# Kernel optimization log

Hardware: AMD Instinct MI355X
Metric: run time of the kernel (lower is better)

Reference implementation:

```python
import jax, jax.numpy as jnp
import numpy as np

ALL_NODE_NUM = 12288
FEA_DIM = 32           # dim2 in DGATNet
BATCH_SIZE = 8
WIN_NUM = 4
POOLED_PER_WIN = 192   # ratio=0.5 of 384 nodes per window graph
N_EDGES = 393216       # avg degree 32


def setup_inputs() -> dict:
    key = jax.random.key(0)
    k1, k2, k3, k4, k5 = jax.random.split(key, 5)
    n_perm = BATCH_SIZE * WIN_NUM * POOLED_PER_WIN  # 6144
    fea = jax.random.normal(k1, (n_perm, FEA_DIM), dtype=jnp.float32)
    # perm: unique sorted node indices kept by the pooling stage
    perm = jnp.sort(jax.random.permutation(k2, ALL_NODE_NUM)[:n_perm]).astype(jnp.int32)
    encoder_edge_index = jax.random.randint(k3, (2, N_EDGES), 0, ALL_NODE_NUM, dtype=jnp.int32)
    encoder_edge_attr = jax.random.uniform(k4, (N_EDGES,), dtype=jnp.float32)
    node_atte_coffe = jax.random.uniform(k5, (BATCH_SIZE * POOLED_PER_WIN,), dtype=jnp.float32)
    return {
        "fea": fea,
        "perm": perm,
        "encoder_edge_index": encoder_edge_index,
        "encoder_edge_attr": encoder_edge_attr,
        "node_atte_coffe": node_atte_coffe,
        "all_node_num": ALL_NODE_NUM,
        "batch_size": BATCH_SIZE,
    }


def reference(fea, perm, encoder_edge_index, encoder_edge_attr, node_atte_coffe,
              all_node_num, batch_size):
    """Faithful JAX translation of DiffusioUnpool.forward (DGATNet.unpool)."""
    n_perm, fea_dim = fea.shape
    slide_win_num = n_perm // node_atte_coffe.shape[0]
    node_num = node_atte_coffe.shape[0] // batch_size

    # ones(B,W,1) @ coffe(B,1,node_num) == tile coefficients over windows
    nac = node_atte_coffe.reshape(batch_size, 1, node_num)
    win_nac = jnp.broadcast_to(nac, (batch_size, slide_win_num, node_num)).reshape(-1)

    # scatter pooled features / coefficients back into the full node set
    x_zero = jnp.zeros((all_node_num, fea_dim), dtype=fea.dtype).at[perm].set(fea)
    atte_zero = jnp.zeros((all_node_num,), dtype=fea.dtype).at[perm].set(win_nac)

    # dense adjacency (duplicate edges sum, as in sparse_coo_tensor + to_dense)
    A = jnp.zeros((all_node_num, all_node_num), dtype=fea.dtype)
    A = A.at[encoder_edge_index[0], encoder_edge_index[1]].add(encoder_edge_attr)
    A = A + jnp.eye(all_node_num, dtype=fea.dtype)  # + I self loops

    d = 1.0 / jnp.sqrt(jnp.sum(A, axis=1))  # diag of D = deg^{-1/2}
    # D A D x  ==  d * (A @ (d * x))
    x = d[:, None] * (A @ (d[:, None] * x_zero))
    atte_updata = d * (A @ (d * atte_zero))
    return x, atte_updata
```

## Files before the change

kernel.cpp:

```cpp
#include <hip/hip_runtime.h>

constexpr int ALL_NODES = 12288;
constexpr int FEA       = 32;
constexpr int N_PERM    = 6144;
constexpr int N_EDGES   = 393216;
constexpr int NODE_NUM  = 192;
constexpr int WINxNODE  = 768;

constexpr int RCAP   = 48;
constexpr int NWORDS = ALL_NODES / 32;

constexpr size_t ROWBUF_OFF = 0;
constexpr size_t YC_OFF   = ROWBUF_OFF + (size_t)ALL_NODES * RCAP * 2;
constexpr size_t CNT_OFF  = YC_OFF + (size_t)N_PERM * FEA;
constexpr size_t DEG_OFF  = CNT_OFF + ALL_NODES;
constexpr size_t DV_OFF   = DEG_OFF + ALL_NODES;
constexpr size_t YA_OFF   = DV_OFF + ALL_NODES;
constexpr size_t BMP_OFF  = YA_OFF + N_PERM;
constexpr size_t RANK_OFF = BMP_OFF + NWORDS;

__global__ __launch_bounds__(512) void k_init(const int* __restrict__ perm,
                                              unsigned int* __restrict__ cnt,
                                              float* __restrict__ deg,
                                              unsigned int* __restrict__ bmp,
                                              int* __restrict__ rank) {
    int t = threadIdx.x;
    if (blockIdx.x == 0) {
        __shared__ int pops[NWORDS];
        unsigned bits = 0u;
        if (t < NWORDS) {
            int base = t * 32;
            int loI = 0, hiI = N_PERM;
            while (loI < hiI) {
                int mid = (loI + hiI) >> 1;
                if (perm[mid] < base) loI = mid + 1; else hiI = mid;
            }
            for (int k = loI; k < N_PERM; ++k) {
                int p = perm[k];
                if (p >= base + 32) break;
                bits |= 1u << (p - base);
            }
            bmp[t] = bits;
            pops[t] = __popc(bits);
        }
        __syncthreads();
        for (int off = 1; off < NWORDS; off <<= 1) {
            int v = 0;
            if (t < NWORDS && t >= off) v = pops[t - off];
            __syncthreads();
            if (t < NWORDS) pops[t] += v;
            __syncthreads();
        }
        if (t < NWORDS) rank[t] = pops[t] - __popc(bits);
    } else {
        int z = (blockIdx.x - 1) * 512 + t;
        if (z < ALL_NODES) cnt[z] = 0u;
        else deg[z - ALL_NODES] = 0.f;
    }
}

__global__ __launch_bounds__(256) void k_bin(const int* __restrict__ ei0,
                                             const int* __restrict__ ei1,
                                             const float* __restrict__ attr,
                                             const unsigned int* __restrict__ bmp,
                                             const int* __restrict__ rank,
                                             float* __restrict__ deg,
                                             unsigned int* __restrict__ cnt,
                                             uint2* __restrict__ rowbuf) {
    int e = blockIdx.x * 256 + threadIdx.x;
    int r = ei0[e];
    int c = ei1[e];
    float w = attr[e];
    atomicAdd(&deg[r], w);
    unsigned word = bmp[c >> 5];
    if ((word >> (c & 31)) & 1u) {
        int kk = rank[c >> 5] + __popc(word & ((1u << (c & 31)) - 1u));
        unsigned slot = atomicAdd(&cnt[r], 1u);
        if (slot < RCAP)
            rowbuf[(size_t)r * RCAP + slot] =
                make_uint2((unsigned)kk, __float_as_uint(w));
    }
}

__global__ __launch_bounds__(256) void k_post(const float* __restrict__ fea,
                                              const float* __restrict__ nac,
                                              const float* __restrict__ deg,
                                              const unsigned int* __restrict__ bmp,
                                              const int* __restrict__ rank,
                                              float* __restrict__ dv,
                                              float* __restrict__ yc,
                                              float* __restrict__ ya) {
    int tg = blockIdx.x * 256 + threadIdx.x;
    int i = tg >> 3, s = tg & 7;
    float d = rsqrtf(1.0f + deg[i]);
    if (s == 0) dv[i] = d;
    unsigned word = bmp[i >> 5];
    if ((word >> (i & 31)) & 1u) {
        int kk = rank[i >> 5] + __popc(word & ((1u << (i & 31)) - 1u));
        float4 v = *(const float4*)(fea + (size_t)kk * FEA + s * 4);
        v.x *= d; v.y *= d; v.z *= d; v.w *= d;
        ((float4*)yc)[(size_t)kk * 8 + s] = v;
        if (s == 0)
            ya[kk] = d * nac[(kk / WINxNODE) * NODE_NUM + (kk % NODE_NUM)];
    }
}

__global__ __launch_bounds__(256) void k_spmv(const uint2* __restrict__ rowbuf,
                                              const unsigned int* __restrict__ cnt,
                                              const float* __restrict__ dv,
                                              const float* __restrict__ yc,
                                              const float* __restrict__ ya,
                                              const unsigned int* __restrict__ bmp,
                                              const int* __restrict__ rank,
                                              float* __restrict__ out_x,
                                              float* __restrict__ out_a) {
    int t = threadIdx.x;
    int r = blockIdx.x * 8 + (t >> 5);
    int f = t & 31;
    int n = (int)cnt[r]; if (n > RCAP) n = RCAP;
    const uint2* rp = rowbuf + (size_t)r * RCAP;
    float acc = 0.f, accA = 0.f;
    int i = 0;
    for (; i + 4 <= n; i += 4) {
        uint2 e0 = rp[i],     e1 = rp[i + 1];
        uint2 e2 = rp[i + 2], e3 = rp[i + 3];
        float y0 = yc[(size_t)e0.x * FEA + f];
        float y1 = yc[(size_t)e1.x * FEA + f];
        float y2 = yc[(size_t)e2.x * FEA + f];
        float y3 = yc[(size_t)e3.x * FEA + f];
        acc += __uint_as_float(e0.y) * y0 + __uint_as_float(e1.y) * y1
             + __uint_as_float(e2.y) * y2 + __uint_as_float(e3.y) * y3;
        if (f == 0)
            accA += __uint_as_float(e0.y) * ya[e0.x]
                  + __uint_as_float(e1.y) * ya[e1.x]
                  + __uint_as_float(e2.y) * ya[e2.x]
                  + __uint_as_float(e3.y) * ya[e3.x];
    }
    for (; i < n; ++i) {
        uint2 e = rp[i];
        acc += __uint_as_float(e.y) * yc[(size_t)e.x * FEA + f];
        if (f == 0) accA += __uint_as_float(e.y) * ya[e.x];
    }
    float d = dv[r];
    unsigned word = bmp[r >> 5];
    float self = 0.f, selfa = 0.f;
    if ((word >> (r & 31)) & 1u) {
        int kk = rank[r >> 5] + __popc(word & ((1u << (r & 31)) - 1u));
        self  = yc[(size_t)kk * FEA + f];
        selfa = ya[kk];
    }
    out_x[(size_t)r * FEA + f] = d * (acc + self);
    if (f == 0)
        out_a[r] = d * (accA + selfa);
}

extern "C" void kernel_launch(void* const* d_in, const int* in_sizes, int n_in,
                              void* d_out, int out_size, void* d_ws, size_t ws_size,
                              hipStream_t stream) {
    const float* fea  = (const float*)d_in[0];
    const int*   perm = (const int*)d_in[1];
    const int*   ei   = (const int*)d_in[2];
    const float* attr = (const float*)d_in[3];
    const float* nac  = (const float*)d_in[4];

    unsigned int* ws     = (unsigned int*)d_ws;
    uint2*        rowbuf = (uint2*)(ws + ROWBUF_OFF);
    float*        yc     = (float*)(ws + YC_OFF);
    unsigned int* cnt    = ws + CNT_OFF;
    float*        deg    = (float*)(ws + DEG_OFF);
    float*        dv     = (float*)(ws + DV_OFF);
    float*        ya     = (float*)(ws + YA_OFF);
    unsigned int* bmp    = ws + BMP_OFF;
    int*          rank   = (int*)(ws + RANK_OFF);

    float* out_x = (float*)d_out;
    float* out_a = out_x + ALL_NODES * FEA;

    k_init<<<49,            512, 0, stream>>>(perm, cnt, deg, bmp, rank);
    k_bin <<<N_EDGES / 256, 256, 0, stream>>>(ei, ei + N_EDGES, attr, bmp, rank,
                                              deg, cnt, rowbuf);
    k_post<<<384,           256, 0, stream>>>(fea, nac, deg, bmp, rank, dv, yc, ya);
    k_spmv<<<ALL_NODES / 8, 256, 0, stream>>>(rowbuf, cnt, dv, yc, ya, bmp, rank,
                                              out_x, out_a);
}
```

Measured before the change: 120.6 us.

## Pack degree and slot count into one 64-bit atomic, drop post kernel

Merges the per-row float degree atomic and the slot-counter atomic into a single 64-bit integer atomicAdd, with the degree held in fixed point in the low 40 bits and the count in the high bits. This halves the atomic traffic in the binning pass. It also removes the separate post kernel that built pre-scaled feature and attention vectors: the SpMV now reads raw features and coefficients and computes the column degree scaling on the fly from the packed counter. The cost is an extra gather of the column's counter per edge, fixed-point rounding of the degrees, and a packed column index with the rank in each rowbuf entry.

```diff
diff --git a/kernel.cpp b/kernel.cpp
--- a/kernel.cpp
+++ b/kernel.cpp
@@ -9,19 +9,16 @@
 
 constexpr int RCAP   = 48;
 constexpr int NWORDS = ALL_NODES / 32;
+constexpr float FIX   = 16777216.0f;
+constexpr float UNFIX = 1.0f / 16777216.0f;
 
-constexpr size_t ROWBUF_OFF = 0;
-constexpr size_t YC_OFF   = ROWBUF_OFF + (size_t)ALL_NODES * RCAP * 2;
-constexpr size_t CNT_OFF  = YC_OFF + (size_t)N_PERM * FEA;
-constexpr size_t DEG_OFF  = CNT_OFF + ALL_NODES;
-constexpr size_t DV_OFF   = DEG_OFF + ALL_NODES;
-constexpr size_t YA_OFF   = DV_OFF + ALL_NODES;
-constexpr size_t BMP_OFF  = YA_OFF + N_PERM;
-constexpr size_t RANK_OFF = BMP_OFF + NWORDS;
+constexpr size_t CNT_OFF    = 0;
+constexpr size_t ROWBUF_OFF = CNT_OFF + 2 * (size_t)ALL_NODES;
+constexpr size_t BMP_OFF    = ROWBUF_OFF + (size_t)ALL_NODES * RCAP * 2;
+constexpr size_t RANK_OFF   = BMP_OFF + NWORDS;
 
 __global__ __launch_bounds__(512) void k_init(const int* __restrict__ perm,
-                                              unsigned int* __restrict__ cnt,
-                                              float* __restrict__ deg,
+                                              unsigned int* __restrict__ cnt_w,
                                               unsigned int* __restrict__ bmp,
                                               int* __restrict__ rank) {
     int t = threadIdx.x;
@@ -53,9 +50,7 @@
         }
         if (t < NWORDS) rank[t] = pops[t] - __popc(bits);
     } else {
-        int z = (blockIdx.x - 1) * 512 + t;
-        if (z < ALL_NODES) cnt[z] = 0u;
-        else deg[z - ALL_NODES] = 0.f;
+        cnt_w[(blockIdx.x - 1) * 512 + t] = 0u;
     }
 }
 
@@ -64,52 +59,37 @@
                                              const float* __restrict__ attr,
                                              const unsigned int* __restrict__ bmp,
                                              const int* __restrict__ rank,
-                                             float* __restrict__ deg,
-                                             unsigned int* __restrict__ cnt,
+                                             unsigned long long* __restrict__ cnt64,
                                              uint2* __restrict__ rowbuf) {
     int e = blockIdx.x * 256 + threadIdx.x;
     int r = ei0[e];
     int c = ei1[e];
     float w = attr[e];
-    atomicAdd(&deg[r], w);
+    unsigned wfix = __float2uint_rn(w * FIX);
     unsigned word = bmp[c >> 5];
-    if ((word >> (c & 31)) & 1u) {
-        int kk = rank[c >> 5] + __popc(word & ((1u << (c & 31)) - 1u));
-        unsigned slot = atomicAdd(&cnt[r], 1u);
-        if (slot < RCAP)
+    bool live = (word >> (c & 31)) & 1u;
+    unsigned long long add = (unsigned long long)wfix
+                           | (live ? (1ULL << 40) : 0ULL);
+    unsigned long long old = atomicAdd(cnt64 + r, add);
+    if (live) {
+        unsigned slot = (unsigned)(old >> 40);
+        if (slot < RCAP) {
+            int kk = rank[c >> 5] + __popc(word & ((1u << (c & 31)) - 1u));
             rowbuf[(size_t)r * RCAP + slot] =
-                make_uint2((unsigned)kk, __float_as_uint(w));
+                make_uint2(((unsigned)kk << 14) | (unsigned)c, __float_as_uint(w));
+        }
     }
 }
 
-__global__ __launch_bounds__(256) void k_post(const float* __restrict__ fea,
-                                              const float* __restrict__ nac,
-                                              const float* __restrict__ deg,
-                                              const unsigned int* __restrict__ bmp,
-                                              const int* __restrict__ rank,
-                                              float* __restrict__ dv,
-                                              float* __restrict__ yc,
-                                              float* __restrict__ ya) {
-    int tg = blockIdx.x * 256 + threadIdx.x;
-    int i = tg >> 3, s = tg & 7;
-    float d = rsqrtf(1.0f + deg[i]);
-    if (s == 0) dv[i] = d;
-    unsigned word = bmp[i >> 5];
-    if ((word >> (i & 31)) & 1u) {
-        int kk = rank[i >> 5] + __popc(word & ((1u << (i & 31)) - 1u));
-        float4 v = *(const float4*)(fea + (size_t)kk * FEA + s * 4);
-        v.x *= d; v.y *= d; v.z *= d; v.w *= d;
-        ((float4*)yc)[(size_t)kk * 8 + s] = v;
-        if (s == 0)
-            ya[kk] = d * nac[(kk / WINxNODE) * NODE_NUM + (kk % NODE_NUM)];
-    }
+__device__ __forceinline__ float deg_to_d(unsigned long long cv) {
+    unsigned dsum = (unsigned)(cv & 0xFFFFFFFFFFULL);
+    return rsqrtf(1.0f + (float)dsum * UNFIX);
 }
 
 __global__ __launch_bounds__(256) void k_spmv(const uint2* __restrict__ rowbuf,
-                                              const unsigned int* __restrict__ cnt,
-                                              const float* __restrict__ dv,
-                                              const float* __restrict__ yc,
-                                              const float* __restrict__ ya,
+                                              const unsigned long long* __restrict__ cnt64,
+                                              const float* __restrict__ fea,
+                                              const float* __restrict__ nac,
                                               const unsigned int* __restrict__ bmp,
                                               const int* __restrict__ rank,
                                               float* __restrict__ out_x,
@@ -117,41 +97,55 @@
     int t = threadIdx.x;
     int r = blockIdx.x * 8 + (t >> 5);
     int f = t & 31;
-    int n = (int)cnt[r]; if (n > RCAP) n = RCAP;
+    unsigned long long cv = cnt64[r];
+    int n = (int)(cv >> 40); if (n > RCAP) n = RCAP;
+    float d_r = deg_to_d(cv);
     const uint2* rp = rowbuf + (size_t)r * RCAP;
     float acc = 0.f, accA = 0.f;
     int i = 0;
     for (; i + 4 <= n; i += 4) {
         uint2 e0 = rp[i],     e1 = rp[i + 1];
         uint2 e2 = rp[i + 2], e3 = rp[i + 3];
-        float y0 = yc[(size_t)e0.x * FEA + f];
-        float y1 = yc[(size_t)e1.x * FEA + f];
-        float y2 = yc[(size_t)e2.x * FEA + f];
-        float y3 = yc[(size_t)e3.x * FEA + f];
-        acc += __uint_as_float(e0.y) * y0 + __uint_as_float(e1.y) * y1
-             + __uint_as_float(e2.y) * y2 + __uint_as_float(e3.y) * y3;
+        int kk0 = e0.x >> 14, c0 = e0.x & 16383;
+        int kk1 = e1.x >> 14, c1 = e1.x & 16383;
+        int kk2 = e2.x >> 14, c2 = e2.x & 16383;
+        int kk3 = e3.x >> 14, c3 = e3.x & 16383;
+        float d0 = deg_to_d(cnt64[c0]);
+        float d1 = deg_to_d(cnt64[c1]);
+        float d2 = deg_to_d(cnt64[c2]);
+        float d3 = deg_to_d(cnt64[c3]);
+        float y0 = fea[(size_t)kk0 * FEA + f];
+        float y1 = fea[(size_t)kk1 * FEA + f];
+        float y2 = fea[(size_t)kk2 * FEA + f];
+        float y3 = fea[(size_t)kk3 * FEA + f];
+        float w0 = __uint_as_float(e0.y), w1 = __uint_as_float(e1.y);
+        float w2 = __uint_as_float(e2.y), w3 = __uint_as_float(e3.y);
+        acc += w0 * d0 * y0 + w1 * d1 * y1 + w2 * d2 * y2 + w3 * d3 * y3;
         if (f == 0)
-            accA += __uint_as_float(e0.y) * ya[e0.x]
-                  + __uint_as_float(e1.y) * ya[e1.x]
-                  + __uint_as_float(e2.y) * ya[e2.x]
-                  + __uint_as_float(e3.y) * ya[e3.x];
+            accA += w0 * d0 * nac[(kk0 / WINxNODE) * NODE_NUM + (kk0 % NODE_NUM)]
+                  + w1 * d1 * nac[(kk1 / WINxNODE) * NODE_NUM + (kk1 % NODE_NUM)]
+                  + w2 * d2 * nac[(kk2 / WINxNODE) * NODE_NUM + (kk2 % NODE_NUM)]
+                  + w3 * d3 * nac[(kk3 / WINxNODE) * NODE_NUM + (kk3 % NODE_NUM)];
     }
     for (; i < n; ++i) {
         uint2 e = rp[i];
-        acc += __uint_as_float(e.y) * yc[(size_t)e.x * FEA + f];
-        if (f == 0) accA += __uint_as_float(e.y) * ya[e.x];
+        int kk = e.x >> 14, c = e.x & 16383;
+        float d = deg_to_d(cnt64[c]);
+        float w = __uint_as_float(e.y);
+        acc += w * d * fea[(size_t)kk * FEA + f];
+        if (f == 0)
+            accA += w * d * nac[(kk / WINxNODE) * NODE_NUM + (kk % NODE_NUM)];
     }
-    float d = dv[r];
     unsigned word = bmp[r >> 5];
     float self = 0.f, selfa = 0.f;
     if ((word >> (r & 31)) & 1u) {
-        int kk = rank[r >> 5] + __popc(word & ((1u << (r & 31)) - 1u));
-        self  = yc[(size_t)kk * FEA + f];
-        selfa = ya[kk];
+        int kkr = rank[r >> 5] + __popc(word & ((1u << (r & 31)) - 1u));
+        self  = d_r * fea[(size_t)kkr * FEA + f];
+        selfa = d_r * nac[(kkr / WINxNODE) * NODE_NUM + (kkr % NODE_NUM)];
     }
-    out_x[(size_t)r * FEA + f] = d * (acc + self);
+    out_x[(size_t)r * FEA + f] = d_r * (acc + self);
     if (f == 0)
-        out_a[r] = d * (accA + selfa);
+        out_a[r] = d_r * (accA + selfa);
 }
 
 extern "C" void kernel_launch(void* const* d_in, const int* in_sizes, int n_in,
@@ -163,23 +157,18 @@
     const float* attr = (const float*)d_in[3];
     const float* nac  = (const float*)d_in[4];
 
-    unsigned int* ws     = (unsigned int*)d_ws;
-    uint2*        rowbuf = (uint2*)(ws + ROWBUF_OFF);
-    float*        yc     = (float*)(ws + YC_OFF);
-    unsigned int* cnt    = ws + CNT_OFF;
-    float*        deg    = (float*)(ws + DEG_OFF);
-    float*        dv     = (float*)(ws + DV_OFF);
-    float*        ya     = (float*)(ws + YA_OFF);
-    unsigned int* bmp    = ws + BMP_OFF;
-    int*          rank   = (int*)(ws + RANK_OFF);
+    unsigned int*       ws     = (unsigned int*)d_ws;
+    unsigned long long* cnt64  = (unsigned long long*)(ws + CNT_OFF);
+    uint2*              rowbuf = (uint2*)(ws + ROWBUF_OFF);
+    unsigned int*       bmp    = ws + BMP_OFF;
+    int*                rank   = (int*)(ws + RANK_OFF);
 
     float* out_x = (float*)d_out;
     float* out_a = out_x + ALL_NODES * FEA;
 
-    k_init<<<49,            512, 0, stream>>>(perm, cnt, deg, bmp, rank);
+    k_init<<<49,            512, 0, stream>>>(perm, (unsigned int*)cnt64, bmp, rank);
     k_bin <<<N_EDGES / 256, 256, 0, stream>>>(ei, ei + N_EDGES, attr, bmp, rank,
-                                              deg, cnt, rowbuf);
-    k_post<<<384,           256, 0, stream>>>(fea, nac, deg, bmp, rank, dv, yc, ya);
-    k_spmv<<<ALL_NODES / 8, 256, 0, stream>>>(rowbuf, cnt, dv, yc, ya, bmp, rank,
+                                              cnt64, rowbuf);
+    k_spmv<<<ALL_NODES / 8, 256, 0, stream>>>(rowbuf, cnt64, fea, nac, bmp, rank,
                                               out_x, out_a);
 }
```

Result: faster. 106.8 us (-11.5%).
